# Performance work log

Hardware: AMD Instinct MI355X
Metric: run time of the kernel (lower is better)

## Reference

```python
import jax, jax.numpy as jnp
import numpy as np

EPS = 1e-10

def _mlp(x, W1, b1, W2, b2):
    # Linear -> ReLU -> Linear (matches _MultiLayerPercep)
    return jnp.maximum(x @ W1 + b1, 0.0) @ W2 + b2

def setup_inputs() -> dict:
    key = jax.random.key(0)
    ks = jax.random.split(key, 24)
    B, P, Q, P2, D = 512, 100, 40, 40, 64
    Nu, Ni, Nr = 100000, 100000, 6

    def lin(k, fi, fo):
        kw, kb = jax.random.split(k)
        s = 1.0 / np.sqrt(fi)
        return (jax.random.uniform(kw, (fi, fo), jnp.float32, -s, s),
                jax.random.uniform(kb, (fo,), jnp.float32, -s, s))

    uids = jax.random.randint(ks[0], (B,), 0, Nu)
    u_item_pad = jnp.stack([jax.random.randint(ks[1], (B, P), 0, Ni),
                            jax.random.randint(ks[2], (B, P), 0, Nr)], axis=-1)
    u_user_pad = jax.random.randint(ks[3], (B, Q), 0, Nu)
    u_user_item_pad = jnp.stack([jax.random.randint(ks[4], (B, Q, P2), 0, Ni),
                                 jax.random.randint(ks[5], (B, Q, P2), 0, Nr)], axis=-1)

    user_table = jax.random.normal(ks[6], (Nu, D), jnp.float32) * 0.1
    item_table = jax.random.normal(ks[7], (Ni, D), jnp.float32) * 0.1
    rate_table = jax.random.normal(ks[8], (Nr, D), jnp.float32) * 0.1

    gv_W1, gv_b1 = lin(ks[9], 2 * D, D)
    gv_W2, gv_b2 = lin(ks[10], D, D)
    atti_W1, atti_b1 = lin(ks[11], 2 * D, D)
    atti_W2, atti_b2 = lin(ks[12], D, 1)
    agg_W, agg_b = lin(ks[13], D, D)
    attu_W1, attu_b1 = lin(ks[14], 2 * D, D)
    attu_W2, attu_b2 = lin(ks[15], D, 1)
    aggn_W, aggn_b = lin(ks[16], D, D)
    cm_W1, cm_b1 = lin(ks[17], 2 * D, D)
    cm_W2, cm_b2 = lin(ks[18], D, D)
    cm_W3, cm_b3 = lin(ks[19], D, D)

    return dict(uids=uids, u_item_pad=u_item_pad, u_user_pad=u_user_pad,
                u_user_item_pad=u_user_item_pad,
                user_table=user_table, item_table=item_table, rate_table=rate_table,
                gv_W1=gv_W1, gv_b1=gv_b1, gv_W2=gv_W2, gv_b2=gv_b2,
                atti_W1=atti_W1, atti_b1=atti_b1, atti_W2=atti_W2, atti_b2=atti_b2,
                agg_W=agg_W, agg_b=agg_b,
                attu_W1=attu_W1, attu_b1=attu_b1, attu_W2=attu_W2, attu_b2=attu_b2,
                aggn_W=aggn_W, aggn_b=aggn_b,
                cm_W1=cm_W1, cm_b1=cm_b1, cm_W2=cm_W2, cm_b2=cm_b2, cm_W3=cm_W3, cm_b3=cm_b3)

def reference(uids, u_item_pad, u_user_pad, u_user_item_pad,
              user_table, item_table, rate_table,
              gv_W1, gv_b1, gv_W2, gv_b2,
              atti_W1, atti_b1, atti_W2, atti_b2,
              agg_W, agg_b,
              attu_W1, attu_b1, attu_W2, attu_b2,
              aggn_W, aggn_b,
              cm_W1, cm_b1, cm_W2, cm_b2, cm_W3, cm_b3):
    f32 = jnp.float32

    # ---- item aggregation branch ----
    q_a = item_table[u_item_pad[:, :, 0]]                      # [B,P,D]
    mask_u = (u_item_pad[:, :, 0] > 0).astype(f32)             # [B,P]
    er = rate_table[u_item_pad[:, :, 1]]                       # [B,P,D]
    x_ia = _mlp(jnp.concatenate([q_a, er], -1), gv_W1, gv_b1, gv_W2, gv_b2)
    p_i = mask_u[..., None] * user_table[uids][:, None, :]     # [B,P,D]
    alpha = _mlp(jnp.concatenate([x_ia, p_i], -1), atti_W1, atti_b1, atti_W2, atti_b2)[..., 0]
    alpha = jnp.exp(alpha) * mask_u
    alpha = alpha / (jnp.sum(alpha, axis=1, keepdims=True) + EPS)
    h_iI = jnp.maximum(jnp.sum(alpha[..., None] * x_ia, axis=1) @ agg_W + agg_b, 0.0)  # [B,D]

    # ---- social branch: per-neighbor item aggregation ----
    q_a_s = item_table[u_user_item_pad[:, :, :, 0]]            # [B,Q,P2,D]
    mask_s = (u_user_item_pad[:, :, :, 0] > 0).astype(f32)     # [B,Q,P2]
    er_s = rate_table[u_user_item_pad[:, :, :, 1]]
    x_ia_s = _mlp(jnp.concatenate([q_a_s, er_s], -1), gv_W1, gv_b1, gv_W2, gv_b2)
    nbr_emb = user_table[u_user_pad]                           # [B,Q,D]
    p_i_s = mask_s[..., None] * nbr_emb[:, :, None, :]
    alpha_s = _mlp(jnp.concatenate([x_ia_s, p_i_s], -1), atti_W1, atti_b1, atti_W2, atti_b2)[..., 0]
    alpha_s = jnp.exp(alpha_s) * mask_s
    alpha_s = alpha_s / (jnp.sum(alpha_s, axis=2, keepdims=True) + EPS)
    h_oI = jnp.maximum(jnp.sum(alpha_s[..., None] * x_ia_s, axis=2) @ agg_W + agg_b, 0.0)  # [B,Q,D]

    # ---- social attention over neighbors ----
    beta = _mlp(jnp.concatenate([h_oI, nbr_emb], -1), attu_W1, attu_b1, attu_W2, attu_b2)[..., 0]
    mask_su = (u_user_pad > 0).astype(f32)
    beta = jnp.exp(beta) * mask_su
    beta = beta / (jnp.sum(beta, axis=1, keepdims=True) + EPS)
    h_iS = jnp.maximum(jnp.sum(beta[..., None] * h_oI, axis=1) @ aggn_W + aggn_b, 0.0)  # [B,D]

    # ---- combine ----
    h = jnp.maximum(jnp.concatenate([h_iI, h_iS], -1) @ cm_W1 + cm_b1, 0.0)
    h = jnp.maximum(h @ cm_W2 + cm_b2, 0.0)
    h = jnp.maximum(h @ cm_W3 + cm_b3, 0.0)
    return h
```

## Files before the change

kernel.cpp:

```cpp
#include <hip/hip_runtime.h>
#include <math.h>

#define EPSV 1e-10f

typedef _Float16 f16x8 __attribute__((ext_vector_type(8)));
typedef _Float16 f16x4 __attribute__((ext_vector_type(4)));
typedef float f32x4 __attribute__((ext_vector_type(4)));

#define OFF_W1T  0
#define OFF_W2T  16384
#define OFF_M2T  24576
#define OFF_U    32768
#define OFF_B1   (32768 + 1024)
#define OFF_V    36864
#define SMEM_SZ  40960

__device__ __forceinline__ f16x8 cvt_f16x8(const float4 a, const float4 b) {
  f16x8 h;
  h[0] = (_Float16)a.x; h[1] = (_Float16)a.y; h[2] = (_Float16)a.z; h[3] = (_Float16)a.w;
  h[4] = (_Float16)b.x; h[5] = (_Float16)b.y; h[6] = (_Float16)b.z; h[7] = (_Float16)b.w;
  return h;
}

__global__ __launch_bounds__(256, 3) void agg_kernel(
    const int nIblk,
    const int* __restrict__ idsS, const int* __restrict__ uidS,
    const int* __restrict__ idsI, const int* __restrict__ uidI,
    const float* __restrict__ user_table, const float* __restrict__ item_table,
    const float* __restrict__ rate_table,
    const float* __restrict__ gv_W1, const float* __restrict__ gv_b1,
    const float* __restrict__ gv_W2, const float* __restrict__ gv_b2,
    const float* __restrict__ atti_W1, const float* __restrict__ atti_b1,
    const float* __restrict__ atti_W2, const float* __restrict__ atti_b2,
    const float* __restrict__ agg_W, const float* __restrict__ agg_b,
    float* __restrict__ outS, float* __restrict__ outI) {
  __shared__ __align__(16) char smem[SMEM_SZ];
  const int tid = threadIdx.x;
  const int wave = tid >> 6, lane = tid & 63;
  const int quad = lane >> 4, mrow = lane & 15;

  const bool isS = (int)blockIdx.x >= nIblk;
  const int NG = isS ? 16 : 4;
  const int P = isS ? 40 : 100;
  const int nGrp = isS ? 4 : 1;
  const int tpg = isS ? 3 : 8;
  const int nIdx = nGrp * tpg;
  const int* __restrict__ ids = isS ? idsS : idsI;
  const int* __restrict__ uidp = isS ? uidS : uidI;
  float* __restrict__ out = isS ? outS : outI;
  const int gbase = isS ? ((int)blockIdx.x - nIblk) * 16 : (int)blockIdx.x * 4;

  float* sV = (float*)(smem + OFF_V);
  char* smXw = smem + OFF_W1T + wave * 4096;
  float* csW = (float*)smXw;

  {
    float* uS = (float*)(smem + OFF_U);
    float* AU = (float*)(smem + OFF_W1T);
    for (int t = tid; t < NG * 64; t += 256) {
      const int g = t >> 6, f = t & 63;
      uS[t] = user_table[(size_t)uidp[gbase + g] * 64 + f];
    }
    for (int o = tid; o < 1024; o += 256) {
      const int k = o >> 4, fb = o & 15;
      const float4 v = ((const float4*)(atti_W1 + (64 + k) * 64))[fb];
      const float* vp = (const float*)&v;
#pragma unroll
      for (int c = 0; c < 4; ++c) {
        const int j = fb * 4 + c;
        AU[j * 64 + (((k >> 2) ^ (j & 15)) << 2) + (k & 3)] = vp[c];
      }
    }
  }
  __syncthreads();
  {
    const float4* u4 = (const float4*)(smem + OFF_U);
    const float4* a4 = (const float4*)(smem + OFF_W1T);
    for (int t = tid; t < NG * 64; t += 256) {
      const int g = t >> 6, j = t & 63;
      float s = 0.f;
#pragma unroll 4
      for (int kb = 0; kb < 16; ++kb) {
        const float4 uu = u4[g * 16 + kb];
        const float4 aa = a4[j * 16 + (kb ^ (j & 15))];
        s += uu.x * aa.x + uu.y * aa.y + uu.z * aa.z + uu.w * aa.w;
      }
      sV[t] = s;
    }
  }
  __syncthreads();
  {
    for (int o = tid; o < 1024; o += 256) {
      const int k = o >> 4, fb = o & 15;
      const float4 v = ((const float4*)(gv_W1 + k * 64))[fb];
      const float* vp = (const float*)&v;
#pragma unroll
      for (int c = 0; c < 4; ++c) {
        const int n = fb * 4 + c;
        *(_Float16*)(smem + OFF_W1T + n * 256 + ((((k >> 3) ^ (n & 7))) << 4) +
                     ((k & 7) << 1)) = (_Float16)vp[c];
      }
    }
    for (int o = tid; o < 1024; o += 256) {
      const int h = o >> 4, fb = o & 15;
      const float4 v = ((const float4*)(gv_W2 + h * 64))[fb];
      const float* vp = (const float*)&v;
#pragma unroll
      for (int c = 0; c < 4; ++c) {
        const int n = fb * 4 + c;
        *(_Float16*)(smem + OFF_W2T + n * 128 + ((((h >> 3) ^ (n & 7))) << 4) +
                     ((h & 7) << 1)) = (_Float16)vp[c];
      }
    }
    for (int o = tid; o < 2048; o += 256) {
      const int r = o >> 6, n = o & 63;
      float s = 0.f;
      if (r < 6) {
#pragma unroll 8
        for (int k = 0; k < 64; ++k)
          s = fmaf(rate_table[r * 64 + k], gv_W1[(64 + k) * 64 + n], s);
      }
      *(_Float16*)(smem + OFF_W1T + n * 256 +
                   (((8 + (r >> 3)) ^ (n & 7)) << 4) + ((r & 7) << 1)) =
          (_Float16)s;
    }
    if (tid < 16) ((float4*)(smem + OFF_B1))[tid] = ((const float4*)gv_b1)[tid];
    float* sCstP = (float*)(smem + OFF_U);
    const int n = tid & 63, jh = tid >> 6;
    float p = 0.f;
#pragma unroll 4
    for (int jj = 0; jj < 16; ++jj) {
      const int j = jh * 16 + jj;
      p = fmaf(gv_b2[j], atti_W1[j * 64 + n], p);
    }
    sCstP[jh * 64 + n] = p;
  }
  float b2v[4], aw2v[4];
#pragma unroll
  for (int nt = 0; nt < 4; ++nt) {
    b2v[nt] = gv_b2[nt * 16 + mrow];
    aw2v[nt] = atti_W2[nt * 16 + mrow];
  }
  const float ab2 = atti_b2[0];

  const int nIdxM1 = nIdx - 1;
  int2 idreg;
  float4 pf[4];
  float pm;
  int rid;
  auto load_ids = [&](int idx) __attribute__((always_inline)) {
    const int ic = idx < nIdxM1 ? idx : nIdxM1;
    const int gq = isS ? (ic * 11) >> 5 : (ic >> 3);
    const int tt = ic - gq * tpg;
    const int it = tt * 16 + mrow;
    int2 pr = make_int2(0, 0);
    if (it < P) {
      const int g2 = gbase + wave + 4 * gq;
      pr = ((const int2*)ids)[(size_t)g2 * P + it];
    }
    idreg = pr;
  };
  auto issue_gather = [&]() __attribute__((always_inline)) {
    const int iid = idreg.x;
    rid = idreg.y;
    pm = iid > 0 ? 1.f : 0.f;
    const float* ib = item_table + (size_t)iid * 64 + quad * 8;
    pf[0] = ((const float4*)ib)[0];
    pf[1] = ((const float4*)ib)[1];
    pf[2] = ((const float4*)(ib + 32))[0];
    pf[3] = ((const float4*)(ib + 32))[1];
  };
  load_ids(0); issue_gather();
  load_ids(1);
  __syncthreads();
  float cstv[4];
  {
    f16x8 aM[2];
#pragma unroll
    for (int ks = 0; ks < 2; ++ks) {
      f16x8 t;
#pragma unroll
      for (int j = 0; j < 8; ++j)
        t[j] = (_Float16)atti_W1[(ks * 32 + quad * 8 + j) * 64 + (wave * 16 + mrow)];
      aM[ks] = t;
    }
#pragma unroll
    for (int ht = 0; ht < 4; ++ht) {
      f32x4 c = {0.f, 0.f, 0.f, 0.f};
#pragma unroll
      for (int ks = 0; ks < 2; ++ks) {
        const float* s = gv_W2 + (ht * 16 + mrow) * 64 + ks * 32 + quad * 8;
        f16x8 b;
#pragma unroll
        for (int j = 0; j < 8; ++j) b[j] = (_Float16)s[j];
        c = __builtin_amdgcn_mfma_f32_16x16x32_f16(aM[ks], b, c, 0, 0, 0);
      }
      const int h = ht * 16 + mrow;
#pragma unroll
      for (int rg = 0; rg < 4; ++rg) {
        const int n3 = wave * 16 + quad * 4 + rg;
        *(_Float16*)(smem + OFF_M2T + n3 * 128 + ((((h >> 3) ^ (n3 & 7))) << 4) +
                     ((h & 7) << 1)) = (_Float16)c[rg];
      }
    }
    const float* sCstP = (const float*)(smem + OFF_U);
#pragma unroll
    for (int nt = 0; nt < 4; ++nt) {
      const int n = nt * 16 + mrow;
      cstv[nt] = atti_b1[n] + sCstP[n] + sCstP[64 + n] + sCstP[128 + n] +
                 sCstP[192 + n];
    }
  }
  __syncthreads();

  f16x8 aW[4][3];
#pragma unroll
  for (int nt = 0; nt < 4; ++nt) {
#pragma unroll
    for (int ks = 0; ks < 3; ++ks)
      aW[nt][ks] = *(const f16x8*)(smem + OFF_W1T + (nt * 16 + mrow) * 256 +
                                   (((ks * 4 + quad) ^ (mrow & 7)) << 4));
  }
  __syncthreads();

  float vv[4], pnum[4], pden = 0.f;
  for (int idx = 0; idx < nIdx; ++idx) {
    const int gq = isS ? (idx * 11) >> 5 : (idx >> 3);
    const int tt = idx - gq * tpg;
    const int g = wave + 4 * gq;
    if (tt == 0) {
#pragma unroll
      for (int nt = 0; nt < 4; ++nt) {
        vv[nt] = sV[g * 64 + nt * 16 + mrow];
        pnum[nt] = 0.f;
      }
      pden = 0.f;
    }
    f16x8 bIn0 = cvt_f16x8(pf[0], pf[1]);
    f16x8 bIn1 = cvt_f16x8(pf[2], pf[3]);
    const float mcur = pm;
    const int ridcur = rid;
    issue_gather();
    load_ids(idx + 2);
    f16x8 bOne;
#pragma unroll
    for (int j = 0; j < 8; ++j)
      bOne[j] = (_Float16)(quad * 8 + j == ridcur ? 1.f : 0.f);
#pragma unroll
    for (int nt = 0; nt < 4; ++nt) {
      f32x4 c = {0.f, 0.f, 0.f, 0.f};
      c = __builtin_amdgcn_mfma_f32_16x16x32_f16(aW[nt][0], bIn0, c, 0, 0, 0);
      c = __builtin_amdgcn_mfma_f32_16x16x32_f16(aW[nt][1], bIn1, c, 0, 0, 0);
      c = __builtin_amdgcn_mfma_f32_16x16x32_f16(aW[nt][2], bOne, c, 0, 0, 0);
      const float4 b1q = *(const float4*)(smem + OFF_B1 + nt * 64 + quad * 16);
      const float* b1p = (const float*)&b1q;
      f16x4 hv;
#pragma unroll
      for (int rg = 0; rg < 4; ++rg)
        hv[rg] = (_Float16)fmaxf(c[rg] + b1p[rg], 0.f);
      *(f16x4*)(smXw + mrow * 256 +
                (((nt * 2 + (quad >> 1)) ^ (mrow & 7)) << 4) +
                ((quad & 1) << 3)) = hv;
    }
    f16x8 a2[2];
#pragma unroll
    for (int ks = 0; ks < 2; ++ks)
      a2[ks] = *(const f16x8*)(smXw + mrow * 256 +
                               (((ks * 4 + quad) ^ (mrow & 7)) << 4));
    float mk[4];
#pragma unroll
    for (int rg = 0; rg < 4; ++rg) mk[rg] = __shfl(mcur, quad * 4 + rg);
    f32x4 x2a[4];
    float tl[4] = {0.f, 0.f, 0.f, 0.f};
#pragma unroll
    for (int nt = 0; nt < 4; ++nt) {
      f32x4 c = {0.f, 0.f, 0.f, 0.f}, d = {0.f, 0.f, 0.f, 0.f};
#pragma unroll
      for (int ks = 0; ks < 2; ++ks) {
        const f16x8 bW = *(const f16x8*)(smem + OFF_W2T + (nt * 16 + mrow) * 128 +
                                         (((ks * 4 + quad) ^ (mrow & 7)) << 4));
        c = __builtin_amdgcn_mfma_f32_16x16x32_f16(a2[ks], bW, c, 0, 0, 0);
      }
#pragma unroll
      for (int ks = 0; ks < 2; ++ks) {
        const f16x8 bM = *(const f16x8*)(smem + OFF_M2T + (nt * 16 + mrow) * 128 +
                                         (((ks * 4 + quad) ^ (mrow & 7)) << 4));
        d = __builtin_amdgcn_mfma_f32_16x16x32_f16(a2[ks], bM, d, 0, 0, 0);
      }
      x2a[nt] = c;
#pragma unroll
      for (int rg = 0; rg < 4; ++rg) {
        const float hh = fmaxf(d[rg] + cstv[nt] + mk[rg] * vv[nt], 0.f);
        tl[rg] = fmaf(hh, aw2v[nt], tl[rg]);
      }
    }
    float e[4];
#pragma unroll
    for (int rg = 0; rg < 4; ++rg) {
      float t = tl[rg];
      t += __shfl_xor(t, 1); t += __shfl_xor(t, 2);
      t += __shfl_xor(t, 4); t += __shfl_xor(t, 8);
      e[rg] = __expf(t + ab2) * mk[rg];
      pden += e[rg];
    }
#pragma unroll
    for (int nt = 0; nt < 4; ++nt) {
      pnum[nt] = fmaf(e[0], x2a[nt][0], pnum[nt]);
      pnum[nt] = fmaf(e[1], x2a[nt][1], pnum[nt]);
      pnum[nt] = fmaf(e[2], x2a[nt][2], pnum[nt]);
      pnum[nt] = fmaf(e[3], x2a[nt][3], pnum[nt]);
    }
    if (tt == tpg - 1) {
      float dsum = pden;
      dsum += __shfl_xor(dsum, 16); dsum += __shfl_xor(dsum, 32);
      const float rd = 1.f / (dsum + EPSV);
#pragma unroll
      for (int nt = 0; nt < 4; ++nt) {
        float s = pnum[nt];
        s += __shfl_xor(s, 16); s += __shfl_xor(s, 32);
        if (quad == 0) csW[nt * 16 + mrow] = (s + b2v[nt] * dsum) * rd;
      }
      float acc = agg_b[lane];
#pragma unroll 8
      for (int k = 0; k < 64; ++k) acc = fmaf(csW[k], agg_W[k * 64 + lane], acc);
      out[(size_t)(gbase + g) * 64 + lane] = fmaxf(acc, 0.f);
    }
  }
}

#define S2_W1T 0
#define S2_X   17408
#define S2_E   26112
#define S2_MSK 26240
#define S2_HB  26368
#define S2_SZ  27904

__global__ __launch_bounds__(128, 2) void stage2_kernel(
    const int* __restrict__ u_user_pad, const float* __restrict__ user_table,
    const float* __restrict__ hoI, const float* __restrict__ hiI,
    const float* __restrict__ attu_W1, const float* __restrict__ attu_b1,
    const float* __restrict__ attu_W2, const float* __restrict__ attu_b2,
    const float* __restrict__ aggn_W, const float* __restrict__ aggn_b,
    const float* __restrict__ cm_W1, const float* __restrict__ cm_b1,
    const float* __restrict__ cm_W2, const float* __restrict__ cm_b2,
    const float* __restrict__ cm_W3, const float* __restrict__ cm_b3,
    float* __restrict__ out) {
  __shared__ __align__(16) char smem[S2_SZ];
  const int tid = threadIdx.x;
  const int wave = tid >> 6, lane = tid & 63;
  const int quad = lane >> 4, mrow = lane & 15;
  const int b = (int)blockIdx.x * 2 + wave;

  char* sW1 = smem + S2_W1T;
  char* sXw = smem + S2_X + wave * 4352;
  float* sE = (float*)(smem + S2_E) + wave * 16;
  float* sM = (float*)(smem + S2_MSK) + wave * 16;
  float* sB = (float*)(smem + S2_HB) + wave * 192;

  for (int o = tid; o < 2048; o += 128) {
    const int k = o >> 4, fb = o & 15;
    const float4 v = ((const float4*)(attu_W1 + k * 64))[fb];
    const float* vp = (const float*)&v;
#pragma unroll
    for (int c = 0; c < 4; ++c) {
      const int n = fb * 4 + c;
      *(_Float16*)(sW1 + n * 272 + ((k >> 3) << 4) + ((k & 7) << 1)) = (_Float16)vp[c];
    }
  }
  float b1v[4], w2v[4];
#pragma unroll
  for (int nt = 0; nt < 4; ++nt) {
    b1v[nt] = attu_b1[nt * 16 + mrow];
    w2v[nt] = attu_W2[nt * 16 + mrow];
  }
  const float b2s = attu_b2[0];

  float4 pa[4], pb[4];
  float msk[4];
  auto pf = [&](int tt) __attribute__((always_inline)) {
#pragma unroll
    for (int k = 0; k < 4; ++k) {
      const int u = lane + (k << 6);
      const int r = u >> 4, bb = u & 15;
      const int q = tt * 16 + r;
      const int qc = q < 40 ? q : 39;
      int uid = 0;
      float m = 0.f;
      if (q < 40) {
        uid = u_user_pad[b * 40 + q];
        m = uid > 0 ? 1.f : 0.f;
      }
      msk[k] = m;
      const float* src = (bb < 8)
                             ? hoI + ((size_t)b * 40 + qc) * 64 + bb * 8
                             : user_table + (size_t)uid * 64 + (bb - 8) * 8;
      pa[k] = ((const float4*)src)[0];
      pb[k] = ((const float4*)src)[1];
    }
  };
  pf(0);
  __syncthreads();

  float numer = 0.f, pden = 0.f;
  for (int tt = 0; tt < 3; ++tt) {
#pragma unroll
    for (int k = 0; k < 4; ++k) {
      const int u = lane + (k << 6);
      const int r = u >> 4, bb = u & 15;
      *(f16x8*)(sXw + r * 272 + (bb << 4)) = cvt_f16x8(pa[k], pb[k]);
      if (bb == 0) sM[r] = msk[k];
    }
    if (tt < 2) pf(tt + 1);
    f16x8 a[4];
#pragma unroll
    for (int ks = 0; ks < 4; ++ks)
      a[ks] = *(const f16x8*)(sXw + mrow * 272 + ((ks * 4 + quad) << 4));
    float mk[4];
#pragma unroll
    for (int rg = 0; rg < 4; ++rg) mk[rg] = sM[quad * 4 + rg];
    float tl[4] = {0.f, 0.f, 0.f, 0.f};
#pragma unroll
    for (int nt = 0; nt < 4; ++nt) {
      f32x4 d = {0.f, 0.f, 0.f, 0.f};
      const int n = nt * 16 + mrow;
#pragma unroll
      for (int ks = 0; ks < 4; ++ks) {
        const f16x8 bW = *(const f16x8*)(sW1 + n * 272 + ((ks * 4 + quad) << 4));
        d = __builtin_amdgcn_mfma_f32_16x16x32_f16(a[ks], bW, d, 0, 0, 0);
      }
#pragma unroll
      for (int rg = 0; rg < 4; ++rg) {
        const float h = fmaxf(d[rg] + b1v[nt], 0.f);
        tl[rg] = fmaf(h, w2v[nt], tl[rg]);
      }
    }
    float e[4];
#pragma unroll
    for (int rg = 0; rg < 4; ++rg) {
      float t = tl[rg];
      t += __shfl_xor(t, 1); t += __shfl_xor(t, 2);
      t += __shfl_xor(t, 4); t += __shfl_xor(t, 8);
      e[rg] = __expf(t + b2s) * mk[rg];
      pden += e[rg];
    }
    if (mrow == 0) {
#pragma unroll
      for (int rg = 0; rg < 4; ++rg) sE[quad * 4 + rg] = e[rg];
    }
#pragma unroll 4
    for (int r = 0; r < 16; ++r) {
      const float er = sE[r];
      const float xv = (float)*(const _Float16*)(sXw + r * 272 + ((lane >> 3) << 4) +
                                                 ((lane & 7) << 1));
      numer = fmaf(er, xv, numer);
    }
  }
  pden += __shfl_xor(pden, 16);
  pden += __shfl_xor(pden, 32);
  const float hagg = numer / (pden + EPSV);

  sB[128 + lane] = hagg;
  sB[lane] = hiI[(size_t)b * 64 + lane];
  float acc = aggn_b[lane];
#pragma unroll 8
  for (int k = 0; k < 64; ++k) acc = fmaf(sB[128 + k], aggn_W[k * 64 + lane], acc);
  sB[64 + lane] = fmaxf(acc, 0.f);
  float c1 = cm_b1[lane];
#pragma unroll 8
  for (int k = 0; k < 128; ++k) c1 = fmaf(sB[k], cm_W1[k * 64 + lane], c1);
  sB[128 + lane] = fmaxf(c1, 0.f);
  float c2 = cm_b2[lane];
#pragma unroll 8
  for (int k = 0; k < 64; ++k) c2 = fmaf(sB[128 + k], cm_W2[k * 64 + lane], c2);
  sB[lane] = fmaxf(c2, 0.f);
  float c3 = cm_b3[lane];
#pragma unroll 8
  for (int k = 0; k < 64; ++k) c3 = fmaf(sB[k], cm_W3[k * 64 + lane], c3);
  out[(size_t)b * 64 + lane] = fmaxf(c3, 0.f);
}

extern "C" void kernel_launch(void* const* d_in, const int* in_sizes, int n_in,
                              void* d_out, int out_size, void* d_ws, size_t ws_size,
                              hipStream_t stream) {
  const int* uids = (const int*)d_in[0];
  const int* u_item_pad = (const int*)d_in[1];
  const int* u_user_pad = (const int*)d_in[2];
  const int* u_user_item_pad = (const int*)d_in[3];
  const float* user_table = (const float*)d_in[4];
  const float* item_table = (const float*)d_in[5];
  const float* rate_table = (const float*)d_in[6];
  const float* gv_W1 = (const float*)d_in[7];
  const float* gv_b1 = (const float*)d_in[8];
  const float* gv_W2 = (const float*)d_in[9];
  const float* gv_b2 = (const float*)d_in[10];
  const float* atti_W1 = (const float*)d_in[11];
  const float* atti_b1 = (const float*)d_in[12];
  const float* atti_W2 = (const float*)d_in[13];
  const float* atti_b2 = (const float*)d_in[14];
  const float* agg_W = (const float*)d_in[15];
  const float* agg_b = (const float*)d_in[16];
  const float* attu_W1 = (const float*)d_in[17];
  const float* attu_b1 = (const float*)d_in[18];
  const float* attu_W2 = (const float*)d_in[19];
  const float* attu_b2 = (const float*)d_in[20];
  const float* aggn_W = (const float*)d_in[21];
  const float* aggn_b = (const float*)d_in[22];
  const float* cm_W1 = (const float*)d_in[23];
  const float* cm_b1 = (const float*)d_in[24];
  const float* cm_W2 = (const float*)d_in[25];
  const float* cm_b2 = (const float*)d_in[26];
  const float* cm_W3 = (const float*)d_in[27];
  const float* cm_b3 = (const float*)d_in[28];
  float* out = (float*)d_out;

  float* hoI = (float*)d_ws;
  float* hiI = hoI + (size_t)512 * 40 * 64;

  agg_kernel<<<128 + 1280, 256, 0, stream>>>(
      128, u_user_item_pad, u_user_pad, u_item_pad, uids,
      user_table, item_table, rate_table,
      gv_W1, gv_b1, gv_W2, gv_b2,
      atti_W1, atti_b1, atti_W2, atti_b2,
      agg_W, agg_b, hoI, hiI);
  stage2_kernel<<<256, 128, 0, stream>>>(u_user_pad, user_table, hoI, hiI,
                                         attu_W1, attu_b1, attu_W2, attu_b2,
                                         aggn_W, aggn_b,
                                         cm_W1, cm_b1, cm_W2, cm_b2, cm_W3, cm_b3,
                                         out);
}
```

Baseline: 266.1 us.

## Replace one-hot rate MFMA with fp32 LDS lookup and defer W2 MFMA to cut registers

The per-rating projection rate_table@W1b is now stored as an fp32 table in shared memory and added per row, rather than folded into the first MFMA through a one-hot fp16 operand. This drops one MFMA per tile and one register-resident weight fragment. The W2 MFMA is moved after the softmax weights are computed, so the x2a accumulators no longer stay live across the attention MLP. Launch bounds rise from 3 to 4 blocks per SIMD to take advantage of the lower register pressure, at the cost of an extra LDS read per tile and a possible tighter register cap that could spill.

```diff
diff --git a/kernel.cpp b/kernel.cpp
--- a/kernel.cpp
+++ b/kernel.cpp
@@ -11,7 +11,8 @@
 #define OFF_W2T  16384
 #define OFF_M2T  24576
 #define OFF_U    32768
-#define OFF_B1   (32768 + 1024)
+#define OFF_B1   33792
+#define OFF_R1   34048
 #define OFF_V    36864
 #define SMEM_SZ  40960
 
@@ -22,7 +23,7 @@
   return h;
 }
 
-__global__ __launch_bounds__(256, 3) void agg_kernel(
+__global__ __launch_bounds__(256, 4) void agg_kernel(
     const int nIblk,
     const int* __restrict__ idsS, const int* __restrict__ uidS,
     const int* __restrict__ idsI, const int* __restrict__ uidI,
@@ -112,17 +113,16 @@
                      ((h & 7) << 1)) = (_Float16)vp[c];
       }
     }
-    for (int o = tid; o < 2048; o += 256) {
-      const int r = o >> 6, n = o & 63;
-      float s = 0.f;
-      if (r < 6) {
+    {
+      float* sR1 = (float*)(smem + OFF_R1);
+      for (int o = tid; o < 384; o += 256) {
+        const int r = o >> 6, n = o & 63;
+        float s = 0.f;
 #pragma unroll 8
         for (int k = 0; k < 64; ++k)
           s = fmaf(rate_table[r * 64 + k], gv_W1[(64 + k) * 64 + n], s);
-      }
-      *(_Float16*)(smem + OFF_W1T + n * 256 +
-                   (((8 + (r >> 3)) ^ (n & 7)) << 4) + ((r & 7) << 1)) =
-          (_Float16)s;
+        sR1[r * 68 + n] = s;
+      }
     }
     if (tid < 16) ((float4*)(smem + OFF_B1))[tid] = ((const float4*)gv_b1)[tid];
     float* sCstP = (float*)(smem + OFF_U);
@@ -213,16 +213,17 @@
   }
   __syncthreads();
 
-  f16x8 aW[4][3];
+  f16x8 aW[4][2];
 #pragma unroll
   for (int nt = 0; nt < 4; ++nt) {
 #pragma unroll
-    for (int ks = 0; ks < 3; ++ks)
+    for (int ks = 0; ks < 2; ++ks)
       aW[nt][ks] = *(const f16x8*)(smem + OFF_W1T + (nt * 16 + mrow) * 256 +
                                    (((ks * 4 + quad) ^ (mrow & 7)) << 4));
   }
   __syncthreads();
 
+  const float* sR1 = (const float*)(smem + OFF_R1);
   float vv[4], pnum[4], pden = 0.f;
   for (int idx = 0; idx < nIdx; ++idx) {
     const int gq = isS ? (idx * 11) >> 5 : (idx >> 3);
@@ -242,22 +243,19 @@
     const int ridcur = rid;
     issue_gather();
     load_ids(idx + 2);
-    f16x8 bOne;
-#pragma unroll
-    for (int j = 0; j < 8; ++j)
-      bOne[j] = (_Float16)(quad * 8 + j == ridcur ? 1.f : 0.f);
 #pragma unroll
     for (int nt = 0; nt < 4; ++nt) {
       f32x4 c = {0.f, 0.f, 0.f, 0.f};
       c = __builtin_amdgcn_mfma_f32_16x16x32_f16(aW[nt][0], bIn0, c, 0, 0, 0);
       c = __builtin_amdgcn_mfma_f32_16x16x32_f16(aW[nt][1], bIn1, c, 0, 0, 0);
-      c = __builtin_amdgcn_mfma_f32_16x16x32_f16(aW[nt][2], bOne, c, 0, 0, 0);
       const float4 b1q = *(const float4*)(smem + OFF_B1 + nt * 64 + quad * 16);
       const float* b1p = (const float*)&b1q;
+      const float4 r1q = *(const float4*)(sR1 + ridcur * 68 + nt * 16 + quad * 4);
+      const float* r1p = (const float*)&r1q;
       f16x4 hv;
 #pragma unroll
       for (int rg = 0; rg < 4; ++rg)
-        hv[rg] = (_Float16)fmaxf(c[rg] + b1p[rg], 0.f);
+        hv[rg] = (_Float16)fmaxf(c[rg] + b1p[rg] + r1p[rg], 0.f);
       *(f16x4*)(smXw + mrow * 256 +
                 (((nt * 2 + (quad >> 1)) ^ (mrow & 7)) << 4) +
                 ((quad & 1) << 3)) = hv;
@@ -270,24 +268,16 @@
     float mk[4];
 #pragma unroll
     for (int rg = 0; rg < 4; ++rg) mk[rg] = __shfl(mcur, quad * 4 + rg);
-    f32x4 x2a[4];
     float tl[4] = {0.f, 0.f, 0.f, 0.f};
 #pragma unroll
     for (int nt = 0; nt < 4; ++nt) {
-      f32x4 c = {0.f, 0.f, 0.f, 0.f}, d = {0.f, 0.f, 0.f, 0.f};
-#pragma unroll
-      for (int ks = 0; ks < 2; ++ks) {
-        const f16x8 bW = *(const f16x8*)(smem + OFF_W2T + (nt * 16 + mrow) * 128 +
-                                         (((ks * 4 + quad) ^ (mrow & 7)) << 4));
-        c = __builtin_amdgcn_mfma_f32_16x16x32_f16(a2[ks], bW, c, 0, 0, 0);
-      }
+      f32x4 d = {0.f, 0.f, 0.f, 0.f};
 #pragma unroll
       for (int ks = 0; ks < 2; ++ks) {
         const f16x8 bM = *(const f16x8*)(smem + OFF_M2T + (nt * 16 + mrow) * 128 +
                                          (((ks * 4 + quad) ^ (mrow & 7)) << 4));
         d = __builtin_amdgcn_mfma_f32_16x16x32_f16(a2[ks], bM, d, 0, 0, 0);
       }
-      x2a[nt] = c;
 #pragma unroll
       for (int rg = 0; rg < 4; ++rg) {
         const float hh = fmaxf(d[rg] + cstv[nt] + mk[rg] * vv[nt], 0.f);
@@ -305,10 +295,17 @@
     }
 #pragma unroll
     for (int nt = 0; nt < 4; ++nt) {
-      pnum[nt] = fmaf(e[0], x2a[nt][0], pnum[nt]);
-      pnum[nt] = fmaf(e[1], x2a[nt][1], pnum[nt]);
-      pnum[nt] = fmaf(e[2], x2a[nt][2], pnum[nt]);
-      pnum[nt] = fmaf(e[3], x2a[nt][3], pnum[nt]);
+      f32x4 c = {0.f, 0.f, 0.f, 0.f};
+#pragma unroll
+      for (int ks = 0; ks < 2; ++ks) {
+        const f16x8 bW = *(const f16x8*)(smem + OFF_W2T + (nt * 16 + mrow) * 128 +
+                                         (((ks * 4 + quad) ^ (mrow & 7)) << 4));
+        c = __builtin_amdgcn_mfma_f32_16x16x32_f16(a2[ks], bW, c, 0, 0, 0);
+      }
+      pnum[nt] = fmaf(e[0], c[0], pnum[nt]);
+      pnum[nt] = fmaf(e[1], c[1], pnum[nt]);
+      pnum[nt] = fmaf(e[2], c[2], pnum[nt]);
+      pnum[nt] = fmaf(e[3], c[3], pnum[nt]);
     }
     if (tt == tpg - 1) {
       float dsum = pden;
```

Measured after the change: 288.6 us. 1.08x slower.
